# Performance work log

Hardware: AMD Instinct MI355X
Metric: run time of the kernel (lower is better)

Reference implementation:

```python
import jax, jax.numpy as jnp
import numpy as np

PI = 3.141592653589793


def _conv2d(x, w, b=None, pad=0, groups=1):
    out = jax.lax.conv_general_dilated(
        x, w, (1, 1), ((pad, pad), (pad, pad)),
        dimension_numbers=('NCHW', 'OIHW', 'NCHW'), feature_group_count=groups)
    if b is not None:
        out = out + b[None, :, None, None]
    return out


def _l2norm(x, eps=1e-12):
    # torch F.normalize(p=2, dim=1)
    n = jnp.sqrt(jnp.sum(x * x, axis=1, keepdims=True))
    return x / jnp.maximum(n, eps)


def dense_sift(x):
    # Kornia DenseSIFTDescriptor defaults: 8 angular bins, 4x4 spatial bins,
    # spatial_bin_size=4, stride=1, padding=1, rootsift=True, clipval=0.2.
    eps = 1e-10
    nbins = 8
    # SpatialGradient('diff', normalized=False) with replicate padding:
    px = jnp.pad(x, ((0, 0), (0, 0), (0, 0), (1, 1)), mode='edge')
    gx = px[..., 2:] - px[..., :-2]
    py = jnp.pad(x, ((0, 0), (0, 0), (1, 1), (0, 0)), mode='edge')
    gy = py[:, :, 2:, :] - py[:, :, :-2, :]
    mag = jnp.sqrt(gx * gx + gy * gy + eps)
    ori = jnp.arctan2(gy, gx + eps) + 2.0 * PI
    o_big = nbins * ori / (2.0 * PI)
    bo0f = jnp.floor(o_big)
    wo1 = o_big - bo0f
    bo0 = jnp.mod(bo0f, nbins)
    bo1 = jnp.mod(bo0 + 1.0, nbins)
    w0 = (1.0 - wo1) * mag
    w1 = wo1 * mag
    bins = jnp.arange(nbins, dtype=x.dtype).reshape(1, nbins, 1, 1)
    # soft-assign gradient magnitude into 8 orientation bins  (B,8,H,W)
    ang = (bo0 == bins) * w0 + (bo1 == bins) * w1
    # AvgPool2d(4, stride=1, pad=2, count_include_pad=True) -> (B,8,H+1,W+1)
    avg_k = jnp.ones((nbins, 1, 4, 4), x.dtype) / 16.0
    pooled = _conv2d(ang, avg_k, pad=2, groups=nbins)
    # PoolingConv: identity-reshape 4x4 kernel, pad=1 -> 16 shifted copies of 8 chans
    B, _, Hp, Wp = pooled.shape
    H, W = Hp - 1, Wp - 1
    pp = jnp.pad(pooled, ((0, 0), (0, 0), (1, 1), (1, 1)))
    shifts = jnp.stack(
        [pp[:, :, i:i + H, j:j + W] for i in range(4) for j in range(4)], axis=2)
    out = shifts.reshape(B, nbins * 16, H, W)  # channel n = d*16 + i*4 + j
    out = jnp.clip(_l2norm(out), 0.0, 0.2)
    out = _l2norm(out)
    # rootsift: sqrt(L1-normalize + eps)
    l1 = jnp.sum(jnp.abs(out), axis=1, keepdims=True)
    return jnp.sqrt(out / jnp.maximum(l1, 1e-12) + eps)


def joint_bilateral_blur(x, guidance, ksize=5, sigma_color=0.1, sigma_space=1.5):
    # Kornia joint_bilateral_blur, border='reflect', color_distance='l1'
    r = ksize // 2
    ax = jnp.arange(ksize, dtype=x.dtype) - r
    g1 = jnp.exp(-(ax * ax) / (2.0 * sigma_space ** 2))
    g1 = g1 / jnp.sum(g1)
    space_k = jnp.outer(g1, g1)
    H, W = x.shape[-2], x.shape[-1]
    px = jnp.pad(x, ((0, 0), (0, 0), (r, r), (r, r)), mode='reflect')
    pg = jnp.pad(guidance, ((0, 0), (0, 0), (r, r), (r, r)), mode='reflect')
    num = jnp.zeros_like(x)
    den = jnp.zeros((x.shape[0], 1, H, W), x.dtype)
    inv = -0.5 / (sigma_color ** 2)
    for dy in range(ksize):
        for dx in range(ksize):
            gw = pg[:, :, dy:dy + H, dx:dx + W]
            cd = jnp.square(jnp.sum(jnp.abs(gw - guidance), axis=1, keepdims=True))
            k = space_k[dy, dx] * jnp.exp(inv * cd)
            num = num + px[:, :, dy:dy + H, dx:dx + W] * k
            den = den + k
    return num / den


def setup_inputs() -> dict:
    key = jax.random.key(0)
    ks = jax.random.split(key, 7)
    B, H, W = 4, 270, 512
    x = jax.random.uniform(ks[0], (B, 1, H, W), dtype=jnp.float32)
    def winit(k, shape):
        fan_in = shape[1] * shape[2] * shape[3]
        return jax.random.normal(k, shape, dtype=jnp.float32) / np.sqrt(fan_in)
    return {
        'x': x,
        'conv1_w': winit(ks[1], (32, 128, 5, 5)),
        'conv1_b': jax.random.normal(ks[2], (32,), dtype=jnp.float32) * 0.01,
        'conv2_w': winit(ks[3], (8, 32, 3, 3)),
        'conv2_b': jax.random.normal(ks[4], (8,), dtype=jnp.float32) * 0.01,
        'conv3_w': winit(ks[5], (2, 8, 5, 5)),
        'conv3_b': jax.random.normal(ks[6], (2,), dtype=jnp.float32) * 0.01,
    }


def reference(x, conv1_w, conv1_b, conv2_w, conv2_b, conv3_w, conv3_b):
    orig = x
    f = dense_sift(x)
    f = jax.nn.relu(_conv2d(f, conv1_w, conv1_b, pad=2))
    f = jax.nn.relu(_conv2d(f, conv2_w, conv2_b, pad=1))
    f = _conv2d(f, conv3_w, conv3_b, pad=2)
    f = joint_bilateral_blur(f, jnp.concatenate([orig, orig], axis=1))
    u = f[:, 0]
    u = jnp.clip((u - u.min()) / (u.max() - u.min() + 1e-6), 0.0, 1.0)
    u = u * (0.436 * 2.0) - 0.436
    v = f[:, 1]
    v = jnp.clip((v - v.min()) / (v.max() - v.min() + 1e-6), 0.0, 1.0)
    v = v * (0.615 * 2.0) - 0.615
    y = orig[:, 0]
    r = y + 1.14 * v
    g = y - 0.396 * u - 0.581 * v
    b = y + 2.029 * u
    return jnp.stack([r, g, b], axis=1)
```

## Files before the change

### kernel.cpp

```cpp
#include <hip/hip_runtime.h>
#include <hip/hip_bf16.h>

typedef __hip_bfloat16 bf16;
typedef __attribute__((ext_vector_type(8))) short short8v;
typedef __attribute__((ext_vector_type(16))) float f32x16;

#define HH 270
#define WW 512
#define BB 4
#define HP 271
#define WP 513
#define NPIX (HH*WW)
#define NPOOL (HP*WP)
#define TWO_PI 6.28318530717958647692f
#define PLANE ((size_t)BB*NPIX*16)

__global__ void k_wprep(const float* __restrict__ w1, const float* __restrict__ w2,
                        const float* __restrict__ w3, short* __restrict__ apack,
                        float* __restrict__ wT2, float* __restrict__ wT3,
                        float* __restrict__ zp) {
    int stride = gridDim.x * blockDim.x;
    int t0 = blockIdx.x * blockDim.x + threadIdx.x;
    for (int i = t0; i < 1024; i += stride) zp[i] = 0.f;
    for (int i = t0; i < 8*25*64*8; i += stride) {
        int idx = i;
        int j    = idx & 7;  idx >>= 3;
        int lane = idx & 63; idx >>= 6;
        int t    = idx % 25;
        int ck   = idx / 25;
        int o = lane & 31;
        int c = ck*16 + (lane >> 5)*8 + j;
        float v = w1[o*3200 + c*25 + t];
        bf16 h = __float2bfloat16(v);
        apack[i] = *reinterpret_cast<short*>(&h);
    }
    for (int i = t0; i < 288*8;  i += stride) { int ck = i >> 3, o = i & 7;  wT2[i] = w2[o*288  + ck]; }
    for (int i = t0; i < 200*2;  i += stride) { int ck = i >> 1, o = i & 1;  wT3[i] = w3[o*200  + ck]; }
}

__global__ __launch_bounds__(256) void k_pool(const float* __restrict__ x,
                                              float* __restrict__ pooled) {
    __shared__ float hist[8][19][20];
    const int tx = threadIdx.x & 15, ty = threadIdx.x >> 4;
    const int j0 = blockIdx.x * 16, i0 = blockIdx.y * 16, b = blockIdx.z;
    const float* xb = x + (size_t)b * NPIX;

    for (int i = threadIdx.x; i < 8*19*20; i += 256) ((float*)hist)[i] = 0.f;
    __syncthreads();

    for (int i = threadIdx.x; i < 361; i += 256) {
        int lh = i / 19, lw = i - lh*19;
        int hh = i0 + lh - 2, ww = j0 + lw - 2;
        if (hh >= 0 && hh < HH && ww >= 0 && ww < WW) {
            float gx = xb[hh*WW + (ww+1 < WW ? ww+1 : WW-1)] - xb[hh*WW + (ww-1 >= 0 ? ww-1 : 0)];
            float gy = xb[(hh+1 < HH ? hh+1 : HH-1)*WW + ww] - xb[(hh-1 >= 0 ? hh-1 : 0)*WW + ww];
            float mag  = sqrtf(gx*gx + gy*gy + 1e-10f);
            float ori  = atan2f(gy, gx + 1e-10f) + TWO_PI;
            float obig = ori * (8.0f / TWO_PI);
            float b0f  = floorf(obig);
            float wo1  = obig - b0f;
            int ib0 = ((int)b0f) & 7;
            int ib1 = (ib0 + 1) & 7;
            hist[ib0][lh][lw] += (1.0f - wo1) * mag;
            hist[ib1][lh][lw] += wo1 * mag;
        }
    }
    __syncthreads();

    int i = i0 + ty, j = j0 + tx;
    if (i < HP && j < WP) {
        float a[8];
        #pragma unroll
        for (int c = 0; c < 8; ++c) a[c] = 0.f;
        #pragma unroll
        for (int di = 0; di < 4; ++di)
            #pragma unroll
            for (int dj = 0; dj < 4; ++dj) {
                #pragma unroll
                for (int c = 0; c < 8; ++c)
                    a[c] += hist[c][ty+di][tx+dj];
            }
        float* pb = pooled + (size_t)b*8*NPOOL + i*WP + j;
        const float s = 1.0f/16.0f;
        #pragma unroll
        for (int c = 0; c < 8; ++c) pb[c*NPOOL] = a[c]*s;
    }
}

__global__ __launch_bounds__(256) void k_feat(const float* __restrict__ pooled,
                                              short* __restrict__ f2) {
    __shared__ float T[8][19][19];
    const int tx = threadIdx.x & 15, ty = threadIdx.x >> 4;
    const int w0 = blockIdx.x * 16, h0 = blockIdx.y * 16, b = blockIdx.z;
    const float* pb = pooled + (size_t)b*8*NPOOL;

    for (int i = threadIdx.x; i < 8*361; i += 256) {
        int c = i / 361; int r = i - c*361; int lh = r / 19, lw = r - lh*19;
        int ph = h0 + lh - 1, pw = w0 + lw - 1;
        float v = 0.f;
        if (ph >= 0 && ph < HP && pw >= 0 && pw < WP)
            v = pb[c*NPOOL + ph*WP + pw];
        T[c][lh][lw] = v;
    }
    __syncthreads();

    float s2 = 0.f;
    #pragma unroll
    for (int c = 0; c < 8; ++c)
        #pragma unroll
        for (int i = 0; i < 4; ++i)
            #pragma unroll
            for (int j = 0; j < 4; ++j) {
                float u = T[c][ty+i][tx+j];
                s2 += u*u;
            }
    float inv1 = 1.0f / fmaxf(sqrtf(s2), 1e-12f);

    float sv2 = 0.f, sv1 = 0.f;
    #pragma unroll
    for (int c = 0; c < 8; ++c)
        #pragma unroll
        for (int i = 0; i < 4; ++i)
            #pragma unroll
            for (int j = 0; j < 4; ++j) {
                float u = T[c][ty+i][tx+j];
                float v = fminf(u*inv1, 0.2f);
                sv2 += v*v; sv1 += v;
            }
    float inv2  = 1.0f / fmaxf(sqrtf(sv2), 1e-12f);
    float invl1 = 1.0f / fmaxf(sv1 * inv2, 1e-12f);

    int outv[64];
    #pragma unroll
    for (int c = 0; c < 8; ++c)
        #pragma unroll
        for (int i = 0; i < 4; ++i)
            #pragma unroll
            for (int jj = 0; jj < 2; ++jj) {
                float u0 = T[c][ty+i][tx+jj*2];
                float u1 = T[c][ty+i][tx+jj*2+1];
                float v0 = fminf(u0*inv1, 0.2f) * inv2;
                float v1 = fminf(u1*inv1, 0.2f) * inv2;
                float fo0 = sqrtf(v0*invl1 + 1e-10f);
                float fo1 = sqrtf(v1*invl1 + 1e-10f);
                bf16 hb0 = __float2bfloat16(fo0);
                bf16 hb1 = __float2bfloat16(fo1);
                unsigned lo = *reinterpret_cast<unsigned short*>(&hb0);
                unsigned hi = *reinterpret_cast<unsigned short*>(&hb1);
                outv[c*8 + i*2 + jj] = (int)(lo | (hi << 16));
            }

    int h = h0 + ty, w = w0 + tx;
    if (h < HH) {
        const size_t pix = (size_t)b*NPIX + h*WW + w;
        #pragma unroll
        for (int ck = 0; ck < 8; ++ck) {
            int4* fb = reinterpret_cast<int4*>(f2 + (size_t)ck*PLANE + pix*16);
            int4 v0, v1;
            v0.x = outv[ck*8+0]; v0.y = outv[ck*8+1]; v0.z = outv[ck*8+2]; v0.w = outv[ck*8+3];
            v1.x = outv[ck*8+4]; v1.y = outv[ck*8+5]; v1.z = outv[ck*8+6]; v1.w = outv[ck*8+7];
            fb[0] = v0; fb[1] = v1;
        }
    }
}

__global__ __launch_bounds__(256) void k_conv1(const short* __restrict__ f2,
        const short* __restrict__ apack, const float* __restrict__ bias,
        short* __restrict__ c1o, const short* __restrict__ zp16) {
    __shared__ short S[4][2][4608];
    const int tid = threadIdx.x;
    const int l   = tid & 63;
    const int wid = tid >> 6;
    const int n      = blockIdx.x;
    const int xcd    = n & 7;
    const int t_     = n >> 3;
    const int within = t_ & 7;
    const int g      = (t_ >> 3)*8 + xcd;
    const int b      = g / 34;
    const int ypair  = g - b*34;
    const int h0     = (ypair*2 + (within >> 2)) * 4;
    const int w0     = (within & 3) * 128;
    const int c32 = l & 31;
    const int ksel = l >> 5;
    const int gw0 = w0 + wid*32 - 2;

    short* Sw0 = &S[wid][0][0];
    short* Sw1 = &S[wid][1][0];

    f32x16 acc0 = {0.f};
    f32x16 acc1 = {0.f};
    f32x16 acc2 = {0.f};
    f32x16 acc3 = {0.f};

    auto STAGE = [&](int ck, short* dstbase) {
        const short* plane = f2 + (size_t)ck*PLANE;
        #pragma unroll
        for (int j = 0; j < 9; ++j) {
            int s  = j*64 + l;
            int pr = s / 72;
            int rem = s - pr*72;
            int px = rem >> 1;
            int half = rem & 1;
            int gh = h0 + pr - 2;
            int gw = gw0 + px;
            const short* src = ((unsigned)gh < (unsigned)HH && (unsigned)gw < (unsigned)WW)
                ? plane + (((size_t)b*HH + gh)*WW + gw)*16 + half*8
                : zp16;
            __builtin_amdgcn_global_load_lds(
                (const __attribute__((address_space(1))) void*)src,
                (__attribute__((address_space(3))) void*)(dstbase + j*512), 16, 0, 0);
        }
    };

    STAGE(0, Sw0);

    for (int ck = 0; ck < 8; ++ck) {
        short* cur = (ck & 1) ? Sw1 : Sw0;
        short* nxt = (ck & 1) ? Sw0 : Sw1;
        if (ck < 7) STAGE(ck + 1, nxt);
        asm volatile("s_waitcnt vmcnt(9)" ::: "memory");

        #pragma unroll
        for (int kx = 0; kx < 5; ++kx) {
            const int px = c32 + kx;
            const short* bp = cur + (size_t)px*16 + (size_t)ksel*8;
            short8v Bf[8];
            #pragma unroll
            for (int pr = 0; pr < 8; ++pr)
                Bf[pr] = *reinterpret_cast<const short8v*>(bp + pr*576);
            #pragma unroll
            for (int ky = 0; ky < 5; ++ky) {
                const short* ap = apack + ((size_t)(ck*25 + ky*5 + kx)*64 + l)*8;
                short8v A = *reinterpret_cast<const short8v*>(ap);
                acc0 = __builtin_amdgcn_mfma_f32_32x32x16_bf16(A, Bf[ky+0], acc0, 0, 0, 0);
                acc1 = __builtin_amdgcn_mfma_f32_32x32x16_bf16(A, Bf[ky+1], acc1, 0, 0, 0);
                acc2 = __builtin_amdgcn_mfma_f32_32x32x16_bf16(A, Bf[ky+2], acc2, 0, 0, 0);
                acc3 = __builtin_amdgcn_mfma_f32_32x32x16_bf16(A, Bf[ky+3], acc3, 0, 0, 0);
            }
        }
        asm volatile("s_waitcnt lgkmcnt(0)" ::: "memory");
    }

    const int px = w0 + wid*32 + c32;
    #pragma unroll
    for (int r = 0; r < 4; ++r) {
        int h = h0 + r;
        if (h < HH) {
            const f32x16& A = (r==0) ? acc0 : (r==1) ? acc1 : (r==2) ? acc2 : acc3;
            const size_t rowbase = ((size_t)b*HH + h)*4;
            #pragma unroll
            for (int q = 0; q < 4; ++q) {
                short4 pk;
                short* pkp = (short*)&pk;
                #pragma unroll
                for (int j = 0; j < 4; ++j) {
                    float v = fmaxf(A[q*4 + j] + bias[q*8 + 4*ksel + j], 0.f);
                    bf16 hb = __float2bfloat16(v);
                    pkp[j] = *reinterpret_cast<short*>(&hb);
                }
                *reinterpret_cast<short4*>(c1o + ((rowbase + q)*WW + px)*8 + ksel*4) = pk;
            }
        }
    }
}

__global__ __launch_bounds__(256) void k_conv2(const short* __restrict__ in,
        const float* __restrict__ wT, const float* __restrict__ bias,
        float* __restrict__ out) {
    __shared__ float tile[8][18][18];
    int tx = threadIdx.x & 15, ty = threadIdx.x >> 4;
    int h0 = blockIdx.y * 16, w0 = blockIdx.x * 16, b = blockIdx.z;
    float acc[8];
    #pragma unroll
    for (int o = 0; o < 8; ++o) acc[o] = 0.f;

    for (int cc = 0; cc < 4; ++cc) {
        __syncthreads();
        for (int t = threadIdx.x; t < 324; t += 256) {
            int lh = t / 18, lw = t - lh*18;
            int gh = h0 + lh - 1, gw = w0 + lw - 1;
            if (gh >= 0 && gh < HH && gw >= 0 && gw < WW) {
                short8v v = *reinterpret_cast<const short8v*>(
                    in + (((size_t)b*HH + gh)*4 + cc)*WW*8 + (size_t)gw*8);
                #pragma unroll
                for (int c = 0; c < 8; ++c) {
                    unsigned u = ((unsigned)(unsigned short)v[c]) << 16;
                    tile[c][lh][lw] = *reinterpret_cast<float*>(&u);
                }
            } else {
                #pragma unroll
                for (int c = 0; c < 8; ++c) tile[c][lh][lw] = 0.f;
            }
        }
        __syncthreads();
        for (int c = 0; c < 8; ++c) {
            #pragma unroll
            for (int ky = 0; ky < 3; ++ky) {
                #pragma unroll
                for (int kx = 0; kx < 3; ++kx) {
                    float v = tile[c][ty+ky][tx+kx];
                    const float* wp = wT + (((cc*8+c)*9) + ky*3 + kx)*8;
                    #pragma unroll
                    for (int o = 0; o < 8; ++o) acc[o] = fmaf(v, wp[o], acc[o]);
                }
            }
        }
    }
    int h = h0 + ty, w = w0 + tx;
    if (h < HH) {
        float* op = out + (size_t)b*8*NPIX + h*WW + w;
        #pragma unroll
        for (int o = 0; o < 8; ++o) op[(size_t)o*NPIX] = fmaxf(acc[o] + bias[o], 0.f);
    }
}

__global__ __launch_bounds__(256) void k_conv3(const float* __restrict__ in,
        const float* __restrict__ wT, const float* __restrict__ bias,
        float* __restrict__ out) {
    __shared__ float tile[8][20][20];
    int tx = threadIdx.x & 15, ty = threadIdx.x >> 4;
    int h0 = blockIdx.y * 16, w0 = blockIdx.x * 16, b = blockIdx.z;
    float acc0 = 0.f, acc1 = 0.f;

    for (int t = threadIdx.x; t < 8*400; t += 256) {
        int c = t / 400; int r = t - c*400; int lh = r / 20, lw = r - lh*20;
        int gh = h0 + lh - 2, gw = w0 + lw - 2;
        float v = 0.f;
        if (gh >= 0 && gh < HH && gw >= 0 && gw < WW)
            v = in[((size_t)(b*8 + c))*NPIX + gh*WW + gw];
        tile[c][lh][lw] = v;
    }
    __syncthreads();
    for (int c = 0; c < 8; ++c) {
        for (int ky = 0; ky < 5; ++ky) {
            #pragma unroll
            for (int kx = 0; kx < 5; ++kx) {
                float v = tile[c][ty+ky][tx+kx];
                const float* wp = wT + ((c*25) + ky*5 + kx)*2;
                acc0 = fmaf(v, wp[0], acc0);
                acc1 = fmaf(v, wp[1], acc1);
            }
        }
    }
    int h = h0 + ty, w = w0 + tx;
    if (h < HH) {
        float* op = out + (size_t)b*2*NPIX + h*WW + w;
        op[0]    = acc0 + bias[0];
        op[NPIX] = acc1 + bias[1];
    }
}

__device__ __forceinline__ int refl(int i, int n) {
    if (i < 0) i = -i;
    if (i >= n) i = 2*n - 2 - i;
    return i;
}

__global__ void k_bilat(const float* __restrict__ c3, const float* __restrict__ x,
                        float* __restrict__ outb) {
    int idx = blockIdx.x * blockDim.x + threadIdx.x;
    if (idx >= BB*NPIX) return;
    int b = idx / NPIX;
    int p = idx - b*NPIX;
    int h = p / WW, w = p - h*WW;
    const float* xb = x + (size_t)b*NPIX;
    const float* f0 = c3 + (size_t)b*2*NPIX;
    const float* f1 = f0 + NPIX;

    float e1 = expf(-1.0f/4.5f), e2 = expf(-4.0f/4.5f);
    float sden = 1.0f + 2.f*e1 + 2.f*e2;
    float g1v[5] = { e2/sden, e1/sden, 1.0f/sden, e1/sden, e2/sden };

    float g = xb[p];
    float num0 = 0.f, num1 = 0.f, den = 0.f;
    #pragma unroll
    for (int dy = 0; dy < 5; ++dy) {
        int hh = refl(h + dy - 2, HH);
        #pragma unroll
        for (int dx = 0; dx < 5; ++dx) {
            int wc = refl(w + dx - 2, WW);
            float gs = xb[hh*WW + wc];
            float d = gs - g;
            float k = g1v[dy] * g1v[dx] * expf(-200.0f * d * d);
            num0 += f0[hh*WW + wc] * k;
            num1 += f1[hh*WW + wc] * k;
            den  += k;
        }
    }
    float invd = 1.0f / den;
    outb[(size_t)b*2*NPIX + p]        = num0 * invd;
    outb[(size_t)b*2*NPIX + NPIX + p] = num1 * invd;
}

__global__ void k_minmax1(const float* __restrict__ blur, float4* __restrict__ partial) {
    float umin = 3.0e38f, umax = -3.0e38f, vmin = 3.0e38f, vmax = -3.0e38f;
    for (int i = blockIdx.x*blockDim.x + threadIdx.x; i < BB*NPIX; i += gridDim.x*blockDim.x) {
        int b = i / NPIX; int p = i - b*NPIX;
        float u = blur[(size_t)b*2*NPIX + p];
        float v = blur[(size_t)b*2*NPIX + NPIX + p];
        umin = fminf(umin, u); umax = fmaxf(umax, u);
        vmin = fminf(vmin, v); vmax = fmaxf(vmax, v);
    }
    #pragma unroll
    for (int off = 32; off > 0; off >>= 1) {
        umin = fminf(umin, __shfl_down(umin, off));
        umax = fmaxf(umax, __shfl_down(umax, off));
        vmin = fminf(vmin, __shfl_down(vmin, off));
        vmax = fmaxf(vmax, __shfl_down(vmax, off));
    }
    __shared__ float4 sm[4];
    int lane = threadIdx.x & 63, wid = threadIdx.x >> 6;
    if (lane == 0) sm[wid] = make_float4(umin, umax, vmin, vmax);
    __syncthreads();
    if (threadIdx.x == 0) {
        float4 r = sm[0];
        for (int k = 1; k < 4; ++k) {
            r.x = fminf(r.x, sm[k].x); r.y = fmaxf(r.y, sm[k].y);
            r.z = fminf(r.z, sm[k].z); r.w = fmaxf(r.w, sm[k].w);
        }
        partial[blockIdx.x] = r;
    }
}

__global__ void k_minmax2(const float4* __restrict__ partial, float* __restrict__ sc) {
    float4 p = partial[threadIdx.x];
    #pragma unroll
    for (int off = 32; off > 0; off >>= 1) {
        p.x = fminf(p.x, __shfl_down(p.x, off));
        p.y = fmaxf(p.y, __shfl_down(p.y, off));
        p.z = fminf(p.z, __shfl_down(p.z, off));
        p.w = fmaxf(p.w, __shfl_down(p.w, off));
    }
    __shared__ float4 sm[2];
    if ((threadIdx.x & 63) == 0) sm[threadIdx.x >> 6] = p;
    __syncthreads();
    if (threadIdx.x == 0) {
        sc[0] = fminf(sm[0].x, sm[1].x);
        sc[1] = fmaxf(sm[0].y, sm[1].y);
        sc[2] = fminf(sm[0].z, sm[1].z);
        sc[3] = fmaxf(sm[0].w, sm[1].w);
    }
}

__global__ void k_final(const float* __restrict__ blur, const float* __restrict__ x,
                        const float* __restrict__ sc, float* __restrict__ out) {
    int idx = blockIdx.x * blockDim.x + threadIdx.x;
    if (idx >= BB*NPIX) return;
    int b = idx / NPIX;
    int p = idx - b*NPIX;
    float umin = sc[0], umax = sc[1], vmin = sc[2], vmax = sc[3];
    float u = blur[(size_t)b*2*NPIX + p];
    float v = blur[(size_t)b*2*NPIX + NPIX + p];
    u = fminf(fmaxf((u - umin) / (umax - umin + 1e-6f), 0.f), 1.f) * 0.872f - 0.436f;
    v = fminf(fmaxf((v - vmin) / (vmax - vmin + 1e-6f), 0.f), 1.f) * 1.23f  - 0.615f;
    float y = x[(size_t)b*NPIX + p];
    out[(size_t)(b*3+0)*NPIX + p] = y + 1.14f*v;
    out[(size_t)(b*3+1)*NPIX + p] = y - 0.396f*u - 0.581f*v;
    out[(size_t)(b*3+2)*NPIX + p] = y + 2.029f*u;
}

extern "C" void kernel_launch(void* const* d_in, const int* in_sizes, int n_in,
                              void* d_out, int out_size, void* d_ws, size_t ws_size,
                              hipStream_t stream) {
    const float* x  = (const float*)d_in[0];
    const float* w1 = (const float*)d_in[1];
    const float* b1 = (const float*)d_in[2];
    const float* w2 = (const float*)d_in[3];
    const float* b2 = (const float*)d_in[4];
    const float* w3 = (const float*)d_in[5];
    const float* b3 = (const float*)d_in[6];
    float* out = (float*)d_out;
    char* ws = (char*)d_ws;

    const size_t POOLED_OFF = 0;
    const size_t X_OFF      = 17795072;
    const size_t Y_OFF      = X_OFF + 141557760;
    const size_t AP_OFF     = Y_OFF + 35389440;
    const size_t WT2_OFF    = AP_OFF + 409600;
    const size_t WT3_OFF    = WT2_OFF + 9216;
    const size_t PART_OFF   = WT3_OFF + 3328;
    const size_t SC_OFF     = PART_OFF + 2048;
    const size_t ZP_OFF     = SC_OFF + 256;

    float*  pooled = (float*)(ws + POOLED_OFF);
    short*  f2     = (short*)(ws + X_OFF);
    float*  c2o    = (float*)(ws + X_OFF);
    float*  c3o    = (float*)(ws + X_OFF + 24000000);
    float*  blur   = (float*)(ws + X_OFF + 32000000);
    short*  c1o    = (short*)(ws + Y_OFF);
    short*  apack  = (short*)(ws + AP_OFF);
    float*  wT2    = (float*)(ws + WT2_OFF);
    float*  wT3    = (float*)(ws + WT3_OFF);
    float4* part   = (float4*)(ws + PART_OFF);
    float*  sc     = (float*)(ws + SC_OFF);
    float*  zp     = (float*)(ws + ZP_OFF);

    k_wprep<<<512, 256, 0, stream>>>(w1, w2, w3, apack, wT2, wT3, zp);

    dim3 pg((WP + 15)/16, (HP + 15)/16, BB);
    k_pool<<<pg, 256, 0, stream>>>(x, pooled);

    dim3 fg(WW/16, (HH + 15)/16, BB);
    k_feat<<<fg, 256, 0, stream>>>(pooled, f2);

    k_conv1<<<1088, 256, 0, stream>>>(f2, apack, b1, c1o, (const short*)zp);

    dim3 cg(WW/16, (HH + 15)/16, BB);
    k_conv2<<<cg, 256, 0, stream>>>(c1o, wT2, b2, c2o);
    k_conv3<<<cg, 256, 0, stream>>>(c2o, wT3, b3, c3o);

    k_bilat<<<(BB*NPIX + 255)/256, 256, 0, stream>>>(c3o, x, blur);
    k_minmax1<<<128, 256, 0, stream>>>(blur, part);
    k_minmax2<<<1, 128, 0, stream>>>(part, sc);
    k_final<<<(BB*NPIX + 255)/256, 256, 0, stream>>>(blur, x, sc, out);
}
```

Baseline: 313.5 us.

## Run conv2 and conv3 on MFMA bf16 with packed weights and bf16 intermediate

Replaces the scalar FP32 shared-memory conv2 and conv3 kernels with MFMA 16x16x32 bf16 kernels. Both read activations directly from global memory in channel-interleaved bf16 layout, and out-of-range taps point at a zero page. Weights are pre-packed into MFMA A-operand layout, with conv2's 8 outputs padded to 16 and conv3's 25 taps grouped into K=32 chunks. The conv2 output is now stored as bf16 interleaved instead of fp32 planar, which halves its memory traffic. In exchange, precision drops to bf16 and much of each MFMA is wasted on zero padding.

```diff
diff --git a/kernel.cpp b/kernel.cpp
--- a/kernel.cpp
+++ b/kernel.cpp
@@ -3,6 +3,7 @@
 
 typedef __hip_bfloat16 bf16;
 typedef __attribute__((ext_vector_type(8))) short short8v;
+typedef __attribute__((ext_vector_type(4))) float f32x4;
 typedef __attribute__((ext_vector_type(16))) float f32x16;
 
 #define HH 270
@@ -17,7 +18,7 @@
 
 __global__ void k_wprep(const float* __restrict__ w1, const float* __restrict__ w2,
                         const float* __restrict__ w3, short* __restrict__ apack,
-                        float* __restrict__ wT2, float* __restrict__ wT3,
+                        short* __restrict__ a2pack, short* __restrict__ a3pack,
                         float* __restrict__ zp) {
     int stride = gridDim.x * blockDim.x;
     int t0 = blockIdx.x * blockDim.x + threadIdx.x;
@@ -34,8 +35,20 @@
         bf16 h = __float2bfloat16(v);
         apack[i] = *reinterpret_cast<short*>(&h);
     }
-    for (int i = t0; i < 288*8;  i += stride) { int ck = i >> 3, o = i & 7;  wT2[i] = w2[o*288  + ck]; }
-    for (int i = t0; i < 200*2;  i += stride) { int ck = i >> 1, o = i & 1;  wT3[i] = w3[o*200  + ck]; }
+    for (int i = t0; i < 9*64*8; i += stride) {
+        int j = i & 7; int l = (i >> 3) & 63; int tap = i >> 9;
+        int o = l & 15; int cin = (l >> 4)*8 + j;
+        float v = (o < 8) ? w2[o*288 + cin*9 + tap] : 0.f;
+        bf16 h = __float2bfloat16(v);
+        a2pack[i] = *reinterpret_cast<short*>(&h);
+    }
+    for (int i = t0; i < 7*64*8; i += stride) {
+        int j = i & 7; int l = (i >> 3) & 63; int grp = i >> 9;
+        int o = l & 15; int tap = grp*4 + (l >> 4);
+        float v = (o < 2 && tap < 25) ? w3[o*200 + j*25 + tap] : 0.f;
+        bf16 h = __float2bfloat16(v);
+        a3pack[i] = *reinterpret_cast<short*>(&h);
+    }
 }
 
 __global__ __launch_bounds__(256) void k_pool(const float* __restrict__ x,
@@ -264,89 +277,111 @@
     }
 }
 
-__global__ __launch_bounds__(256) void k_conv2(const short* __restrict__ in,
-        const float* __restrict__ wT, const float* __restrict__ bias,
-        float* __restrict__ out) {
-    __shared__ float tile[8][18][18];
-    int tx = threadIdx.x & 15, ty = threadIdx.x >> 4;
-    int h0 = blockIdx.y * 16, w0 = blockIdx.x * 16, b = blockIdx.z;
-    float acc[8];
-    #pragma unroll
-    for (int o = 0; o < 8; ++o) acc[o] = 0.f;
-
-    for (int cc = 0; cc < 4; ++cc) {
-        __syncthreads();
-        for (int t = threadIdx.x; t < 324; t += 256) {
-            int lh = t / 18, lw = t - lh*18;
-            int gh = h0 + lh - 1, gw = w0 + lw - 1;
-            if (gh >= 0 && gh < HH && gw >= 0 && gw < WW) {
-                short8v v = *reinterpret_cast<const short8v*>(
-                    in + (((size_t)b*HH + gh)*4 + cc)*WW*8 + (size_t)gw*8);
-                #pragma unroll
-                for (int c = 0; c < 8; ++c) {
-                    unsigned u = ((unsigned)(unsigned short)v[c]) << 16;
-                    tile[c][lh][lw] = *reinterpret_cast<float*>(&u);
-                }
-            } else {
-                #pragma unroll
-                for (int c = 0; c < 8; ++c) tile[c][lh][lw] = 0.f;
-            }
-        }
-        __syncthreads();
-        for (int c = 0; c < 8; ++c) {
-            #pragma unroll
-            for (int ky = 0; ky < 3; ++ky) {
-                #pragma unroll
-                for (int kx = 0; kx < 3; ++kx) {
-                    float v = tile[c][ty+ky][tx+kx];
-                    const float* wp = wT + (((cc*8+c)*9) + ky*3 + kx)*8;
-                    #pragma unroll
-                    for (int o = 0; o < 8; ++o) acc[o] = fmaf(v, wp[o], acc[o]);
-                }
-            }
-        }
-    }
-    int h = h0 + ty, w = w0 + tx;
-    if (h < HH) {
-        float* op = out + (size_t)b*8*NPIX + h*WW + w;
-        #pragma unroll
-        for (int o = 0; o < 8; ++o) op[(size_t)o*NPIX] = fmaxf(acc[o] + bias[o], 0.f);
-    }
-}
-
-__global__ __launch_bounds__(256) void k_conv3(const float* __restrict__ in,
-        const float* __restrict__ wT, const float* __restrict__ bias,
-        float* __restrict__ out) {
-    __shared__ float tile[8][20][20];
-    int tx = threadIdx.x & 15, ty = threadIdx.x >> 4;
-    int h0 = blockIdx.y * 16, w0 = blockIdx.x * 16, b = blockIdx.z;
-    float acc0 = 0.f, acc1 = 0.f;
-
-    for (int t = threadIdx.x; t < 8*400; t += 256) {
-        int c = t / 400; int r = t - c*400; int lh = r / 20, lw = r - lh*20;
-        int gh = h0 + lh - 2, gw = w0 + lw - 2;
-        float v = 0.f;
-        if (gh >= 0 && gh < HH && gw >= 0 && gw < WW)
-            v = in[((size_t)(b*8 + c))*NPIX + gh*WW + gw];
-        tile[c][lh][lw] = v;
-    }
-    __syncthreads();
-    for (int c = 0; c < 8; ++c) {
-        for (int ky = 0; ky < 5; ++ky) {
-            #pragma unroll
-            for (int kx = 0; kx < 5; ++kx) {
-                float v = tile[c][ty+ky][tx+kx];
-                const float* wp = wT + ((c*25) + ky*5 + kx)*2;
-                acc0 = fmaf(v, wp[0], acc0);
-                acc1 = fmaf(v, wp[1], acc1);
-            }
-        }
-    }
-    int h = h0 + ty, w = w0 + tx;
-    if (h < HH) {
-        float* op = out + (size_t)b*2*NPIX + h*WW + w;
-        op[0]    = acc0 + bias[0];
-        op[NPIX] = acc1 + bias[1];
+__global__ __launch_bounds__(256) void k_conv2m(const short* __restrict__ c1o,
+        const short* __restrict__ a2pack, const float* __restrict__ bias,
+        short* __restrict__ c2o, const short* __restrict__ zp16) {
+    const int tid = threadIdx.x;
+    const int l   = tid & 63;
+    const int wid = tid >> 6;
+    const int h   = blockIdx.y;
+    const int b   = blockIdx.z;
+    const int w0  = blockIdx.x*256 + wid*64;
+    const int col = l & 15;
+    const int kg  = l >> 4;
+
+    f32x4 acc0 = {0.f,0.f,0.f,0.f};
+    f32x4 acc1 = {0.f,0.f,0.f,0.f};
+    f32x4 acc2 = {0.f,0.f,0.f,0.f};
+    f32x4 acc3 = {0.f,0.f,0.f,0.f};
+
+    #pragma unroll
+    for (int ky = 0; ky < 3; ++ky) {
+        int gh = h + ky - 1;
+        bool rv = ((unsigned)gh < (unsigned)HH);
+        const short* rowb = c1o + (((size_t)b*HH + (rv ? gh : 0))*4 + kg)*WW*8;
+        #pragma unroll
+        for (int kx = 0; kx < 3; ++kx) {
+            short8v A = *reinterpret_cast<const short8v*>(
+                a2pack + ((size_t)(ky*3 + kx)*64 + l)*8);
+            #pragma unroll
+            for (int nt = 0; nt < 4; ++nt) {
+                int gw = w0 + nt*16 + col + kx - 1;
+                const short* src = (rv && (unsigned)gw < (unsigned)WW)
+                    ? rowb + (size_t)gw*8 : zp16;
+                short8v B = *reinterpret_cast<const short8v*>(src);
+                if (nt == 0) acc0 = __builtin_amdgcn_mfma_f32_16x16x32_bf16(A, B, acc0, 0, 0, 0);
+                if (nt == 1) acc1 = __builtin_amdgcn_mfma_f32_16x16x32_bf16(A, B, acc1, 0, 0, 0);
+                if (nt == 2) acc2 = __builtin_amdgcn_mfma_f32_16x16x32_bf16(A, B, acc2, 0, 0, 0);
+                if (nt == 3) acc3 = __builtin_amdgcn_mfma_f32_16x16x32_bf16(A, B, acc3, 0, 0, 0);
+            }
+        }
+    }
+
+    if (kg < 2) {
+        #pragma unroll
+        for (int nt = 0; nt < 4; ++nt) {
+            const f32x4& A = (nt==0) ? acc0 : (nt==1) ? acc1 : (nt==2) ? acc2 : acc3;
+            int px = w0 + nt*16 + col;
+            short4 pk;
+            short* pkp = (short*)&pk;
+            #pragma unroll
+            for (int r = 0; r < 4; ++r) {
+                float v = fmaxf(A[r] + bias[kg*4 + r], 0.f);
+                bf16 hb = __float2bfloat16(v);
+                pkp[r] = *reinterpret_cast<short*>(&hb);
+            }
+            *reinterpret_cast<short4*>(c2o + (((size_t)b*HH + h)*WW + px)*8 + kg*4) = pk;
+        }
+    }
+}
+
+__global__ __launch_bounds__(256) void k_conv3m(const short* __restrict__ c2o,
+        const short* __restrict__ a3pack, const float* __restrict__ bias,
+        float* __restrict__ c3o, const short* __restrict__ zp16) {
+    const int tid = threadIdx.x;
+    const int l   = tid & 63;
+    const int wid = tid >> 6;
+    const int h   = blockIdx.y;
+    const int b   = blockIdx.z;
+    const int w0  = blockIdx.x*256 + wid*64;
+    const int col = l & 15;
+    const int kg  = l >> 4;
+
+    f32x4 acc0 = {0.f,0.f,0.f,0.f};
+    f32x4 acc1 = {0.f,0.f,0.f,0.f};
+    f32x4 acc2 = {0.f,0.f,0.f,0.f};
+    f32x4 acc3 = {0.f,0.f,0.f,0.f};
+
+    #pragma unroll
+    for (int grp = 0; grp < 7; ++grp) {
+        int tap = grp*4 + kg;
+        int ky = tap / 5, kx = tap - ky*5;
+        int gh = h + ky - 2;
+        bool tv = (tap < 25) && ((unsigned)gh < (unsigned)HH);
+        const short* rowb = c2o + ((size_t)b*HH + (tv ? gh : 0))*WW*8;
+        short8v A = *reinterpret_cast<const short8v*>(
+            a3pack + ((size_t)grp*64 + l)*8);
+        #pragma unroll
+        for (int nt = 0; nt < 4; ++nt) {
+            int gw = w0 + nt*16 + col + kx - 2;
+            const short* src = (tv && (unsigned)gw < (unsigned)WW)
+                ? rowb + (size_t)gw*8 : zp16;
+            short8v B = *reinterpret_cast<const short8v*>(src);
+            if (nt == 0) acc0 = __builtin_amdgcn_mfma_f32_16x16x32_bf16(A, B, acc0, 0, 0, 0);
+            if (nt == 1) acc1 = __builtin_amdgcn_mfma_f32_16x16x32_bf16(A, B, acc1, 0, 0, 0);
+            if (nt == 2) acc2 = __builtin_amdgcn_mfma_f32_16x16x32_bf16(A, B, acc2, 0, 0, 0);
+            if (nt == 3) acc3 = __builtin_amdgcn_mfma_f32_16x16x32_bf16(A, B, acc3, 0, 0, 0);
+        }
+    }
+
+    if (kg == 0) {
+        #pragma unroll
+        for (int nt = 0; nt < 4; ++nt) {
+            const f32x4& A = (nt==0) ? acc0 : (nt==1) ? acc1 : (nt==2) ? acc2 : acc3;
+            int px = w0 + nt*16 + col;
+            c3o[((size_t)b*2 + 0)*NPIX + h*WW + px] = A[0] + bias[0];
+            c3o[((size_t)b*2 + 1)*NPIX + h*WW + px] = A[1] + bias[1];
+        }
     }
 }
 
@@ -476,26 +511,26 @@
     const size_t X_OFF      = 17795072;
     const size_t Y_OFF      = X_OFF + 141557760;
     const size_t AP_OFF     = Y_OFF + 35389440;
-    const size_t WT2_OFF    = AP_OFF + 409600;
-    const size_t WT3_OFF    = WT2_OFF + 9216;
-    const size_t PART_OFF   = WT3_OFF + 3328;
+    const size_t A2_OFF     = AP_OFF + 204800;
+    const size_t A3_OFF     = A2_OFF + 9216;
+    const size_t PART_OFF   = A3_OFF + 7168;
     const size_t SC_OFF     = PART_OFF + 2048;
     const size_t ZP_OFF     = SC_OFF + 256;
 
     float*  pooled = (float*)(ws + POOLED_OFF);
     short*  f2     = (short*)(ws + X_OFF);
-    float*  c2o    = (float*)(ws + X_OFF);
+    short*  c2o    = (short*)(ws + X_OFF);
     float*  c3o    = (float*)(ws + X_OFF + 24000000);
     float*  blur   = (float*)(ws + X_OFF + 32000000);
     short*  c1o    = (short*)(ws + Y_OFF);
     short*  apack  = (short*)(ws + AP_OFF);
-    float*  wT2    = (float*)(ws + WT2_OFF);
-    float*  wT3    = (float*)(ws + WT3_OFF);
+    short*  a2p    = (short*)(ws + A2_OFF);
+    short*  a3p    = (short*)(ws + A3_OFF);
     float4* part   = (float4*)(ws + PART_OFF);
     float*  sc     = (float*)(ws + SC_OFF);
     float*  zp     = (float*)(ws + ZP_OFF);
 
-    k_wprep<<<512, 256, 0, stream>>>(w1, w2, w3, apack, wT2, wT3, zp);
+    k_wprep<<<512, 256, 0, stream>>>(w1, w2, w3, apack, a2p, a3p, zp);
 
     dim3 pg((WP + 15)/16, (HP + 15)/16, BB);
     k_pool<<<pg, 256, 0, stream>>>(x, pooled);
@@ -505,9 +540,9 @@
 
     k_conv1<<<1088, 256, 0, stream>>>(f2, apack, b1, c1o, (const short*)zp);
 
-    dim3 cg(WW/16, (HH + 15)/16, BB);
-    k_conv2<<<cg, 256, 0, stream>>>(c1o, wT2, b2, c2o);
-    k_conv3<<<cg, 256, 0, stream>>>(c2o, wT3, b3, c3o);
+    dim3 c2g(WW/256, HH, BB);
+    k_conv2m<<<c2g, 256, 0, stream>>>(c1o, a2p, b2, c2o, (const short*)zp);
+    k_conv3m<<<c2g, 256, 0, stream>>>(c2o, a3p, b3, c3o, (const short*)zp);
 
     k_bilat<<<(BB*NPIX + 255)/256, 256, 0, stream>>>(c3o, x, blur);
     k_minmax1<<<128, 256, 0, stream>>>(blur, part);
```

New measurement: 290.5 us. 1.08x faster.
